# Optimization experiments

Hardware: AMD Instinct MI355X
Metric: run time of the kernel (lower is better)

Reference implementation:

```python
import jax, jax.numpy as jnp
import numpy as np

UNITS = 1024
INPUT_DIM = 512
BATCH = 2048

def setup_inputs() -> dict:
    key = jax.random.key(0)
    k1, k2, k3, k4 = jax.random.split(key, 4)
    return {
        "inputs": jax.random.normal(k1, (BATCH, INPUT_DIM), dtype=jnp.float32),
        "h_tm1": jax.random.normal(k2, (BATCH, UNITS), dtype=jnp.float32),
        "c_tm1": jax.random.normal(k3, (BATCH, UNITS), dtype=jnp.float32),
        # keras 'random_normal' initializer: stddev 0.05
        "kernel": jax.random.normal(k4, (UNITS + INPUT_DIM, 4 * UNITS), dtype=jnp.float32) * 0.05,
    }

def reference(inputs, h_tm1, c_tm1, kernel):
    # z = concat([h, x]) @ kernel ; kernel rows: [units (h-block); input_dim (x-block)]
    z = jnp.concatenate([h_tm1, inputs], axis=-1) @ kernel  # [B, 4*units]
    z0, z1, z2, z3 = jnp.split(z, 4, axis=-1)
    i = jax.nn.sigmoid(z0)
    f = jax.nn.sigmoid(z1)
    c_tilde = jnp.tanh(z2)
    o = jax.nn.sigmoid(z3)
    c = f * c_tm1 + i * c_tilde
    h = o * jnp.tanh(c)
    return (h, c)
```

## Files before the change

kernel.cpp:

```cpp
#include <hip/hip_runtime.h>
#include <hip/hip_bf16.h>
#include <stdint.h>

#define UNITS 1024
#define IDIM  512
#define BATCH 2048
#define KTOT  1536
#define NGATE 4096
#define BK    64
#define NITER (KTOT / BK)

typedef short bf16x8 __attribute__((ext_vector_type(8)));
typedef float f32x4  __attribute__((ext_vector_type(4)));

#define AS3(p) ((__attribute__((address_space(3))) void*)(p))
#define AS1(p) ((const __attribute__((address_space(1))) void*)(p))

union P8 { bf16x8 v; __hip_bfloat16 e[8]; };

#define NBLK_A 1536
#define NBLK_T 3072

__global__ __launch_bounds__(256) void prep(
    const float* __restrict__ x, const float* __restrict__ h,
    const float* __restrict__ W,
    __hip_bfloat16* __restrict__ A, __hip_bfloat16* __restrict__ Wt) {
  __shared__ float tile[32][65];
  const int tid = threadIdx.x;
  if (blockIdx.x < NBLK_A) {
    const int id = blockIdx.x * 256 + tid;
    const int r = id / (KTOT / 8);
    const int k = (id % (KTOT / 8)) * 8;
    const float* src = (k < UNITS) ? h + (size_t)r * UNITS + k
                                   : x + (size_t)r * IDIM + (k - UNITS);
    const float4 v0 = ((const float4*)src)[0];
    const float4 v1 = ((const float4*)src)[1];
    P8 o;
    o.e[0] = __float2bfloat16(v0.x); o.e[1] = __float2bfloat16(v0.y);
    o.e[2] = __float2bfloat16(v0.z); o.e[3] = __float2bfloat16(v0.w);
    o.e[4] = __float2bfloat16(v1.x); o.e[5] = __float2bfloat16(v1.y);
    o.e[6] = __float2bfloat16(v1.z); o.e[7] = __float2bfloat16(v1.w);
    *(bf16x8*)(A + (size_t)r * KTOT + k) = o.v;
  } else {
    const int b  = blockIdx.x - NBLK_A;
    const int kb = b >> 7;
    const int nb = b & 127;
    const int k0 = kb * 64, n0 = nb * 32;
    const int n4 = (tid & 7) * 4;
    const int kk = tid >> 3;
#pragma unroll
    for (int rr = 0; rr < 64; rr += 32) {
      const float4 v = *(const float4*)(W + (size_t)(k0 + kk + rr) * NGATE + n0 + n4);
      tile[n4 + 0][kk + rr] = v.x; tile[n4 + 1][kk + rr] = v.y;
      tile[n4 + 2][kk + rr] = v.z; tile[n4 + 3][kk + rr] = v.w;
    }
    __syncthreads();
    const int n  = tid >> 3;
    const int k8 = (tid & 7) * 8;
    P8 o;
#pragma unroll
    for (int j = 0; j < 8; ++j) o.e[j] = __float2bfloat16(tile[n][k8 + j]);
    *(bf16x8*)(Wt + (size_t)(n0 + n) * KTOT + k0 + k8) = o.v;
  }
}

__global__ __launch_bounds__(256, 3) void lstm_gemm(
    const __hip_bfloat16* __restrict__ A,
    const __hip_bfloat16* __restrict__ Wt,
    const float* __restrict__ c_tm1,
    float* __restrict__ out) {
  __shared__ __attribute__((aligned(128))) char lds[3 * 16384];

  const int tid  = threadIdx.x;
  const int w    = tid >> 6;
  const int lane = tid & 63;
  const int quad = lane >> 4;
  const int m16  = lane & 15;
  const int wr   = w >> 1;
  const int wu   = w & 1;

  const int mb = blockIdx.x >> 5;
  const int ub = blockIdx.x & 31;
  const int m0 = mb * 128;
  const int u0 = ub * 32;

  const __hip_bfloat16* aptr[4];
  const __hip_bfloat16* bptr[4];
  int adst[4], bdst[4];
#pragma unroll
  for (int s = 0; s < 4; ++s) {
    const int q   = s * 4 + w;
    const int ci  = q * 64 + lane;
    const int row = ci >> 3;
    const int k8  = (ci & 7) ^ (row & 7);
    aptr[s] = A + (size_t)(m0 + row) * KTOT + k8 * 8;
    adst[s] = q * 1024;
    const int wrow = ((row >> 5) << 10) + u0 + (row & 31);
    bptr[s] = Wt + (size_t)wrow * KTOT + k8 * 8;
    bdst[s] = 32768 + q * 1024;
  }

  f32x4 acc[4][4];
#pragma unroll
  for (int i = 0; i < 4; ++i)
#pragma unroll
    for (int g = 0; g < 4; ++g) {
      f32x4 z = {0.f, 0.f, 0.f, 0.f};
      acc[i][g] = z;
    }

#pragma unroll
  for (int s = 0; s < 4; ++s) {
    __builtin_amdgcn_global_load_lds(AS1(aptr[s]), AS3(lds + adst[s]), 16, 0, 0);
    __builtin_amdgcn_global_load_lds(AS1(bptr[s]), AS3(lds + bdst[s]), 16, 0, 0);
  }
  __syncthreads();

  for (int it = 0; it < NITER; ++it) {
    const int cur = it & 1;
    const int nxt = cur ^ 1;

    bf16x8 breg[4][2];
#pragma unroll
    for (int g = 0; g < 4; ++g)
#pragma unroll
      for (int t = 0; t < 2; ++t) {
        const int vr   = g * 32 + wu * 16 + m16;
        const int slot = (t * 4 + quad) ^ (vr & 7);
        breg[g][t] = *(const bf16x8*)(lds + 32768 + (vr * 8 + slot) * 16);
      }
    __syncthreads();

    if (it < NITER - 1) {
      const int koff = (it + 1) * BK;
#pragma unroll
      for (int s = 0; s < 4; ++s) {
        __builtin_amdgcn_global_load_lds(AS1(aptr[s] + koff),
                                         AS3(lds + nxt * 16384 + adst[s]), 16, 0, 0);
        __builtin_amdgcn_global_load_lds(AS1(bptr[s] + koff),
                                         AS3(lds + bdst[s]), 16, 0, 0);
      }
    }

    const char* abuf = lds + cur * 16384;
#pragma unroll
    for (int t = 0; t < 2; ++t) {
      bf16x8 a[4];
#pragma unroll
      for (int i = 0; i < 4; ++i) {
        const int row  = wr * 64 + i * 16 + m16;
        const int slot = (t * 4 + quad) ^ (row & 7);
        a[i] = *(const bf16x8*)(abuf + (row * 8 + slot) * 16);
      }
#pragma unroll
      for (int g = 0; g < 4; ++g)
#pragma unroll
        for (int i = 0; i < 4; ++i)
          acc[i][g] = __builtin_amdgcn_mfma_f32_16x16x32_bf16(a[i], breg[g][t],
                                                              acc[i][g], 0, 0, 0);
    }
    __syncthreads();
  }

  const int u = u0 + wu * 16 + m16;
#pragma unroll
  for (int i = 0; i < 4; ++i)
#pragma unroll
    for (int reg = 0; reg < 4; ++reg) {
      const int r = m0 + wr * 64 + i * 16 + quad * 4 + reg;
      const float z0 = acc[i][0][reg];
      const float z1 = acc[i][1][reg];
      const float z2 = acc[i][2][reg];
      const float z3 = acc[i][3][reg];
      const float ig = 1.f / (1.f + __expf(-z0));
      const float fg = 1.f / (1.f + __expf(-z1));
      const float ct = 1.f - 2.f / (__expf(2.f * z2) + 1.f);
      const float og = 1.f / (1.f + __expf(-z3));
      const float cc = fg * c_tm1[(size_t)r * UNITS + u] + ig * ct;
      const float hh = og * (1.f - 2.f / (__expf(2.f * cc) + 1.f));
      out[(size_t)r * UNITS + u] = hh;
      out[(size_t)BATCH * UNITS + (size_t)r * UNITS + u] = cc;
    }
}

__global__ __launch_bounds__(256) void lstm_naive(
    const float* __restrict__ x, const float* __restrict__ h,
    const float* __restrict__ c_tm1, const float* __restrict__ W,
    float* __restrict__ out) {
  int idx = blockIdx.x * 256 + threadIdx.x;
  int r = idx / UNITS;
  int u = idx % UNITS;
  float z[4] = {0.f, 0.f, 0.f, 0.f};
  for (int k = 0; k < KTOT; ++k) {
    float a = (k < UNITS) ? h[(size_t)r * UNITS + k] : x[(size_t)r * IDIM + k - UNITS];
#pragma unroll
    for (int g = 0; g < 4; ++g)
      z[g] += a * W[(size_t)k * NGATE + g * UNITS + u];
  }
  float ig = 1.f / (1.f + __expf(-z[0]));
  float fg = 1.f / (1.f + __expf(-z[1]));
  float ct = 1.f - 2.f / (__expf(2.f * z[2]) + 1.f);
  float og = 1.f / (1.f + __expf(-z[3]));
  float cc = fg * c_tm1[(size_t)r * UNITS + u] + ig * ct;
  float hh = og * (1.f - 2.f / (__expf(2.f * cc) + 1.f));
  out[(size_t)r * UNITS + u] = hh;
  out[(size_t)BATCH * UNITS + (size_t)r * UNITS + u] = cc;
}

extern "C" void kernel_launch(void* const* d_in, const int* in_sizes, int n_in,
                              void* d_out, int out_size, void* d_ws, size_t ws_size,
                              hipStream_t stream) {
  const float* x = (const float*)d_in[0];
  const float* h = (const float*)d_in[1];
  const float* c = (const float*)d_in[2];
  const float* W = (const float*)d_in[3];
  float* out = (float*)d_out;

  const size_t needA  = (size_t)BATCH * KTOT * sizeof(__hip_bfloat16);
  const size_t needWt = (size_t)NGATE * KTOT * sizeof(__hip_bfloat16);
  if (ws_size < needA + needWt) {
    hipLaunchKernelGGL(lstm_naive, dim3((BATCH * UNITS) / 256), dim3(256), 0, stream,
                       x, h, c, W, out);
    return;
  }

  __hip_bfloat16* A  = (__hip_bfloat16*)d_ws;
  __hip_bfloat16* Wt = (__hip_bfloat16*)((char*)d_ws + needA);

  hipLaunchKernelGGL(prep, dim3(NBLK_A + NBLK_T), dim3(256), 0, stream, x, h, W, A, Wt);
  hipLaunchKernelGGL(lstm_gemm, dim3(512), dim3(256), 0, stream, A, Wt, c, out);
}
```

Baseline: 125.9 us.

## Halve GEMM M-tile, double-buffer B tile, and prefetch c_tm1 before main loop

The M tile per block shrinks from 128 to 64 rows, doubling the grid to 1024 blocks so more of the chip is busy. The B tile becomes double-buffered in LDS, which removes the register staging of B and the extra barrier in each iteration. c_tm1 is loaded into registers before the K loop so its latency is hidden during the GEMM. In exchange, each block reuses less data from the larger tiles, so total global and L2 traffic for W rises.

```diff
diff --git a/kernel.cpp b/kernel.cpp
--- a/kernel.cpp
+++ b/kernel.cpp
@@ -69,7 +69,7 @@
     const __hip_bfloat16* __restrict__ Wt,
     const float* __restrict__ c_tm1,
     float* __restrict__ out) {
-  __shared__ __attribute__((aligned(128))) char lds[3 * 16384];
+  __shared__ __attribute__((aligned(128))) char lds[49152];
 
   const int tid  = threadIdx.x;
   const int w    = tid >> 6;
@@ -81,28 +81,45 @@
 
   const int mb = blockIdx.x >> 5;
   const int ub = blockIdx.x & 31;
-  const int m0 = mb * 128;
+  const int m0 = mb * 64;
   const int u0 = ub * 32;
 
-  const __hip_bfloat16* aptr[4];
+  const __hip_bfloat16* aptr[2];
   const __hip_bfloat16* bptr[4];
-  int adst[4], bdst[4];
-#pragma unroll
-  for (int s = 0; s < 4; ++s) {
+  int adst[2], bdst[4];
+#pragma unroll
+  for (int s = 0; s < 2; ++s) {
     const int q   = s * 4 + w;
     const int ci  = q * 64 + lane;
     const int row = ci >> 3;
     const int k8  = (ci & 7) ^ (row & 7);
     aptr[s] = A + (size_t)(m0 + row) * KTOT + k8 * 8;
     adst[s] = q * 1024;
+  }
+#pragma unroll
+  for (int s = 0; s < 4; ++s) {
+    const int q   = s * 4 + w;
+    const int ci  = q * 64 + lane;
+    const int row = ci >> 3;
+    const int k8  = (ci & 7) ^ (row & 7);
     const int wrow = ((row >> 5) << 10) + u0 + (row & 31);
     bptr[s] = Wt + (size_t)wrow * KTOT + k8 * 8;
-    bdst[s] = 32768 + q * 1024;
-  }
-
-  f32x4 acc[4][4];
-#pragma unroll
-  for (int i = 0; i < 4; ++i)
+    bdst[s] = 16384 + q * 1024;
+  }
+
+  const int u = u0 + wu * 16 + m16;
+  float cpre[8];
+#pragma unroll
+  for (int i = 0; i < 2; ++i)
+#pragma unroll
+    for (int reg = 0; reg < 4; ++reg) {
+      const int r = m0 + wr * 32 + i * 16 + quad * 4 + reg;
+      cpre[i * 4 + reg] = c_tm1[(size_t)r * UNITS + u];
+    }
+
+  f32x4 acc[2][4];
+#pragma unroll
+  for (int i = 0; i < 2; ++i)
 #pragma unroll
     for (int g = 0; g < 4; ++g) {
       f32x4 z = {0.f, 0.f, 0.f, 0.f};
@@ -110,64 +127,58 @@
     }
 
 #pragma unroll
-  for (int s = 0; s < 4; ++s) {
+  for (int s = 0; s < 2; ++s)
     __builtin_amdgcn_global_load_lds(AS1(aptr[s]), AS3(lds + adst[s]), 16, 0, 0);
+#pragma unroll
+  for (int s = 0; s < 4; ++s)
     __builtin_amdgcn_global_load_lds(AS1(bptr[s]), AS3(lds + bdst[s]), 16, 0, 0);
-  }
   __syncthreads();
 
   for (int it = 0; it < NITER; ++it) {
     const int cur = it & 1;
     const int nxt = cur ^ 1;
-
-    bf16x8 breg[4][2];
-#pragma unroll
-    for (int g = 0; g < 4; ++g)
-#pragma unroll
-      for (int t = 0; t < 2; ++t) {
-        const int vr   = g * 32 + wu * 16 + m16;
-        const int slot = (t * 4 + quad) ^ (vr & 7);
-        breg[g][t] = *(const bf16x8*)(lds + 32768 + (vr * 8 + slot) * 16);
-      }
-    __syncthreads();
-
     if (it < NITER - 1) {
       const int koff = (it + 1) * BK;
 #pragma unroll
-      for (int s = 0; s < 4; ++s) {
+      for (int s = 0; s < 2; ++s)
         __builtin_amdgcn_global_load_lds(AS1(aptr[s] + koff),
-                                         AS3(lds + nxt * 16384 + adst[s]), 16, 0, 0);
+                                         AS3(lds + adst[s] + nxt * 8192), 16, 0, 0);
+#pragma unroll
+      for (int s = 0; s < 4; ++s)
         __builtin_amdgcn_global_load_lds(AS1(bptr[s] + koff),
-                                         AS3(lds + bdst[s]), 16, 0, 0);
-      }
-    }
-
-    const char* abuf = lds + cur * 16384;
+                                         AS3(lds + bdst[s] + nxt * 16384), 16, 0, 0);
+    }
+    const char* abuf = lds + cur * 8192;
+    const char* bbuf = lds + 16384 + cur * 16384;
 #pragma unroll
     for (int t = 0; t < 2; ++t) {
-      bf16x8 a[4];
-#pragma unroll
-      for (int i = 0; i < 4; ++i) {
-        const int row  = wr * 64 + i * 16 + m16;
+      bf16x8 a[2], b[4];
+#pragma unroll
+      for (int i = 0; i < 2; ++i) {
+        const int row  = wr * 32 + i * 16 + m16;
         const int slot = (t * 4 + quad) ^ (row & 7);
         a[i] = *(const bf16x8*)(abuf + (row * 8 + slot) * 16);
       }
 #pragma unroll
+      for (int g = 0; g < 4; ++g) {
+        const int vr   = g * 32 + wu * 16 + m16;
+        const int slot = (t * 4 + quad) ^ (vr & 7);
+        b[g] = *(const bf16x8*)(bbuf + (vr * 8 + slot) * 16);
+      }
+#pragma unroll
       for (int g = 0; g < 4; ++g)
 #pragma unroll
-        for (int i = 0; i < 4; ++i)
-          acc[i][g] = __builtin_amdgcn_mfma_f32_16x16x32_bf16(a[i], breg[g][t],
-                                                              acc[i][g], 0, 0, 0);
+        for (int i = 0; i < 2; ++i)
+          acc[i][g] = __builtin_amdgcn_mfma_f32_16x16x32_bf16(a[i], b[g], acc[i][g], 0, 0, 0);
     }
     __syncthreads();
   }
 
-  const int u = u0 + wu * 16 + m16;
-#pragma unroll
-  for (int i = 0; i < 4; ++i)
+#pragma unroll
+  for (int i = 0; i < 2; ++i)
 #pragma unroll
     for (int reg = 0; reg < 4; ++reg) {
-      const int r = m0 + wr * 64 + i * 16 + quad * 4 + reg;
+      const int r = m0 + wr * 32 + i * 16 + quad * 4 + reg;
       const float z0 = acc[i][0][reg];
       const float z1 = acc[i][1][reg];
       const float z2 = acc[i][2][reg];
@@ -176,7 +187,7 @@
       const float fg = 1.f / (1.f + __expf(-z1));
       const float ct = 1.f - 2.f / (__expf(2.f * z2) + 1.f);
       const float og = 1.f / (1.f + __expf(-z3));
-      const float cc = fg * c_tm1[(size_t)r * UNITS + u] + ig * ct;
+      const float cc = fg * cpre[i * 4 + reg] + ig * ct;
       const float hh = og * (1.f - 2.f / (__expf(2.f * cc) + 1.f));
       out[(size_t)r * UNITS + u] = hh;
       out[(size_t)BATCH * UNITS + (size_t)r * UNITS + u] = cc;
@@ -228,5 +239,5 @@
   __hip_bfloat16* Wt = (__hip_bfloat16*)((char*)d_ws + needA);
 
   hipLaunchKernelGGL(prep, dim3(NBLK_A + NBLK_T), dim3(256), 0, stream, x, h, W, A, Wt);
-  hipLaunchKernelGGL(lstm_gemm, dim3(512), dim3(256), 0, stream, A, Wt, c, out);
-}
+  hipLaunchKernelGGL(lstm_gemm, dim3(1024), dim3(256), 0, stream, A, Wt, c, out);
+}
```

Result: slower. 129.4 us (+2.8%).
